# Kernel tuning notes

Hardware: AMD Instinct MI355X
Metric: run time of the kernel (lower is better)

Reference implementation:

```python
import jax, jax.numpy as jnp
import numpy as np

D = 2048          # latent_dim
H = 4096          # hrm_hidden_dim
K = 4             # hrm_update_interval
MAX_STEPS = 64    # hrm_max_steps
MOM = 0.9         # hrm_momentum
THR = 0.01        # hrm_convergence_threshold


def _gru(x, h, Wih, Whh, bih, bhh):
    # PyTorch GRUCell, gate order r, z, n
    gi = Wih @ x + bih
    gh = Whh @ h + bhh
    ir, iz, inn = jnp.split(gi, 3)
    hr, hz, hn = jnp.split(gh, 3)
    r = jax.nn.sigmoid(ir + hr)
    z = jax.nn.sigmoid(iz + hz)
    n = jnp.tanh(inn + r * hn)
    return (1.0 - z) * n + z * h


def setup_inputs() -> dict:
    key = jax.random.key(0)
    ks = jax.random.split(key, 11)
    f32 = jnp.float32
    def w(k, shape, fan):
        # scaled init (~= torch default 1/sqrt(fan)) so sigmoids/tanh stay in range
        return jax.random.normal(k, shape, f32) / np.float32(np.sqrt(fan))
    return {
        "query":   jax.random.normal(ks[0], (D,), f32),
        "hg_Wih":  w(ks[1], (3 * H, 2 * D), 2 * D),
        "hg_Whh":  w(ks[2], (3 * H, H), H),
        "hg_bih":  jnp.zeros((3 * H,), f32),
        "hg_bhh":  jnp.zeros((3 * H,), f32),
        "hd_W":    w(ks[3], (D, H), H),
        "hd_b":    jnp.zeros((D,), f32),
        "hc_W":    w(ks[4], (1, H), H),
        "hc_b":    jnp.zeros((1,), f32),
        "lg_Wih":  w(ks[5], (3 * D, D), D),
        "lg_Whh":  w(ks[6], (3 * D, D), D),
        "lg_bih":  jnp.zeros((3 * D,), f32),
        "lg_bhh":  jnp.zeros((3 * D,), f32),
        "lo_W":    w(ks[7], (D, D), D),
        "lo_b":    jnp.zeros((D,), f32),
        "halt_W":  w(ks[8], (1, H + D), H + D),
        "halt_b":  jnp.zeros((1,), f32),
        "reset_W": w(ks[9], (1, H + D + 1), H + D + 1),
        "reset_b": jnp.zeros((1,), f32),
        "li_W":    w(ks[10], (D, H), H),
        "li_b":    jnp.zeros((D,), f32),
    }


def reference(query, hg_Wih, hg_Whh, hg_bih, hg_bhh, hd_W, hd_b, hc_W, hc_b,
              lg_Wih, lg_Whh, lg_bih, lg_bhh, lo_W, lo_b,
              halt_W, halt_b, reset_W, reset_b, li_W, li_b):
    q = query[:D]  # reason() truncates/pads flattened query to D

    def step_fn(carry, step):
        h, l, cum, result, rw, mom, best, active, last_res = carry
        # H-module update every K steps (gated by 'active' = not yet halted)
        upd = active & (step % K == 0)
        h_new = _gru(jnp.concatenate([q, l]), h, hg_Wih, hg_Whh, hg_bih, hg_bhh)
        h = jnp.where(upd, h_new, h)
        directive = jnp.tanh(hd_W @ h + hd_b)
        raw_conv = jax.nn.sigmoid(hc_W @ h + hc_b)[0]
        mom = jnp.where(active, MOM * mom + (1.0 - MOM) * raw_conv, mom)
        conv = mom
        # L-module update every step
        l_new = _gru(directive, l, lg_Wih, lg_Whh, lg_bih, lg_bhh)
        l = jnp.where(active, l_new, l)
        res = jnp.tanh(lo_W @ l + lo_b)
        # ACT halting
        halt = jax.nn.sigmoid(halt_W @ jnp.concatenate([h, l]) + halt_b)[0]
        p = jnp.where(active, jnp.minimum(halt, 1.0 - cum), 0.0)
        result = result + p * res
        rw = rw + p
        cum = cum + p
        best = jnp.where(active & (conv > best + THR), conv, best)
        converged = cum > 0.95
        # learned reset (only if not converged this step, and step > K)
        reset_in = jnp.concatenate([h, l, conv[None]])
        reset_p = jax.nn.sigmoid(reset_W @ reset_in + reset_b)[0]
        do_reset = active & (~converged) & (reset_p > 0.7) & (step > K)
        l = jnp.where(do_reset, jnp.tanh(li_W @ h + li_b), l)
        last_res = jnp.where(active, res, last_res)
        active = active & (~converged)
        return (h, l, cum, result, rw, mom, best, active, last_res), None

    f32 = jnp.float32
    init = (jnp.zeros((H,), f32), jnp.zeros((D,), f32), jnp.float32(0.0),
            jnp.zeros((D,), f32), jnp.float32(0.0), jnp.float32(0.0),
            jnp.float32(0.0), jnp.array(True), jnp.zeros((D,), f32))
    (h, l, cum, result, rw, mom, best, active, last_res), _ = jax.lax.scan(
        step_fn, init, jnp.arange(MAX_STEPS))
    # final normalization: result / clamp(result_weight, 1e-8), fallback to last res
    out = jnp.where(rw > 0.0, result / jnp.maximum(rw, 1e-8), last_res)
    return out
```

## Files before the change

### kernel.cpp

```cpp
#include <hip/hip_runtime.h>

static constexpr int D = 2048;
static constexpr int H = 4096;
static constexpr int KSTEP = 4;
static constexpr int MAX_STEPS = 64;
static constexpr float MOMC = 0.9f;

static constexpr int GRID = 256;
static constexpr int BLOCK = 512;

static constexpr int BAR_OFF_FLOATS = 57344;

struct Params {
  const float* query;
  const float* hg_Wih; const float* hg_Whh; const float* hg_bih; const float* hg_bhh;
  const float* hd_W; const float* hd_b;
  const float* hc_W; const float* hc_b;
  const float* lg_Wih; const float* lg_Whh; const float* lg_bih; const float* lg_bhh;
  const float* lo_W; const float* lo_b;
  const float* halt_W; const float* halt_b;
  const float* reset_W; const float* reset_b;
  const float* li_W; const float* li_b;
  float* ws; float* out;
};

__device__ __forceinline__ float sigmoidf_(float x) { return 1.f / (1.f + expf(-x)); }

__device__ __forceinline__ void cstore(float* p, float v) {
  __hip_atomic_store(p, v, __ATOMIC_RELAXED, __HIP_MEMORY_SCOPE_AGENT);
}
__device__ __forceinline__ float cload(const float* p) {
  return __hip_atomic_load(p, __ATOMIC_RELAXED, __HIP_MEMORY_SCOPE_AGENT);
}

__device__ __forceinline__ void gridbar(unsigned* bar, unsigned& mygen) {
  __syncthreads();
  if (threadIdx.x == 0) {
    unsigned* leaf = bar + (blockIdx.x & 15) * 32;
    unsigned* root = bar + 16 * 32;
    unsigned* gen  = bar + 17 * 32;
    const unsigned leafcnt = gridDim.x >> 4;
    const unsigned want = mygen + 1;
    unsigned old = __hip_atomic_fetch_add(leaf, 1u, __ATOMIC_RELEASE, __HIP_MEMORY_SCOPE_AGENT);
    if (old == leafcnt - 1u) {
      __hip_atomic_store(leaf, 0u, __ATOMIC_RELAXED, __HIP_MEMORY_SCOPE_AGENT);
      unsigned ro = __hip_atomic_fetch_add(root, 1u, __ATOMIC_ACQ_REL, __HIP_MEMORY_SCOPE_AGENT);
      if (ro == 15u) {
        __hip_atomic_store(root, 0u, __ATOMIC_RELAXED, __HIP_MEMORY_SCOPE_AGENT);
        __hip_atomic_store(gen, want, __ATOMIC_RELEASE, __HIP_MEMORY_SCOPE_AGENT);
      } else {
        while (__hip_atomic_load(gen, __ATOMIC_RELAXED, __HIP_MEMORY_SCOPE_AGENT) != want)
          __builtin_amdgcn_s_sleep(2);
      }
    } else {
      while (__hip_atomic_load(gen, __ATOMIC_RELAXED, __HIP_MEMORY_SCOPE_AGENT) != want)
        __builtin_amdgcn_s_sleep(2);
    }
  }
  mygen += 1;
  __syncthreads();
}

__device__ __forceinline__ float wred(float v) {
  #pragma unroll
  for (int off = 1; off < 64; off <<= 1) v += __shfl_xor(v, off, 64);
  return v;
}

__device__ __forceinline__ float dot8(const float* __restrict__ row,
                                      const float* __restrict__ vec, int lane) {
  float4 a[8];
  #pragma unroll
  for (int g = 0; g < 8; ++g)
    a[g] = *reinterpret_cast<const float4*>(row + g * 256 + lane * 4);
  float s0 = 0.f, s1 = 0.f, s2 = 0.f, s3 = 0.f;
  #pragma unroll
  for (int g = 0; g < 8; g += 4) {
    float4 b0 = *reinterpret_cast<const float4*>(vec + (g + 0) * 256 + lane * 4);
    float4 b1 = *reinterpret_cast<const float4*>(vec + (g + 1) * 256 + lane * 4);
    float4 b2 = *reinterpret_cast<const float4*>(vec + (g + 2) * 256 + lane * 4);
    float4 b3 = *reinterpret_cast<const float4*>(vec + (g + 3) * 256 + lane * 4);
    s0 = fmaf(a[g+0].x, b0.x, s0); s0 = fmaf(a[g+0].y, b0.y, s0);
    s0 = fmaf(a[g+0].z, b0.z, s0); s0 = fmaf(a[g+0].w, b0.w, s0);
    s1 = fmaf(a[g+1].x, b1.x, s1); s1 = fmaf(a[g+1].y, b1.y, s1);
    s1 = fmaf(a[g+1].z, b1.z, s1); s1 = fmaf(a[g+1].w, b1.w, s1);
    s2 = fmaf(a[g+2].x, b2.x, s2); s2 = fmaf(a[g+2].y, b2.y, s2);
    s2 = fmaf(a[g+2].z, b2.z, s2); s2 = fmaf(a[g+2].w, b2.w, s2);
    s3 = fmaf(a[g+3].x, b3.x, s3); s3 = fmaf(a[g+3].y, b3.y, s3);
    s3 = fmaf(a[g+3].w, b3.w, s3); s3 = fmaf(a[g+3].z, b3.z, s3);
  }
  return (s0 + s1) + (s2 + s3);
}

__device__ __forceinline__ void dot8x2(const float* __restrict__ r0,
                                       const float* __restrict__ r1,
                                       const float* __restrict__ vec,
                                       int lane, float& o0, float& o1) {
  float4 a[8], c[8];
  #pragma unroll
  for (int g = 0; g < 8; ++g)
    a[g] = *reinterpret_cast<const float4*>(r0 + g * 256 + lane * 4);
  #pragma unroll
  for (int g = 0; g < 8; ++g)
    c[g] = *reinterpret_cast<const float4*>(r1 + g * 256 + lane * 4);
  float s0 = 0.f, s1 = 0.f, s2 = 0.f, s3 = 0.f;
  float t0 = 0.f, t1 = 0.f, t2 = 0.f, t3 = 0.f;
  #pragma unroll
  for (int g = 0; g < 8; g += 4) {
    float4 b0 = *reinterpret_cast<const float4*>(vec + (g + 0) * 256 + lane * 4);
    float4 b1 = *reinterpret_cast<const float4*>(vec + (g + 1) * 256 + lane * 4);
    float4 b2 = *reinterpret_cast<const float4*>(vec + (g + 2) * 256 + lane * 4);
    float4 b3 = *reinterpret_cast<const float4*>(vec + (g + 3) * 256 + lane * 4);
    s0 = fmaf(a[g+0].x, b0.x, s0); s0 = fmaf(a[g+0].y, b0.y, s0);
    s0 = fmaf(a[g+0].z, b0.z, s0); s0 = fmaf(a[g+0].w, b0.w, s0);
    s1 = fmaf(a[g+1].x, b1.x, s1); s1 = fmaf(a[g+1].y, b1.y, s1);
    s1 = fmaf(a[g+1].z, b1.z, s1); s1 = fmaf(a[g+1].w, b1.w, s1);
    s2 = fmaf(a[g+2].x, b2.x, s2); s2 = fmaf(a[g+2].y, b2.y, s2);
    s2 = fmaf(a[g+2].z, b2.z, s2); s2 = fmaf(a[g+2].w, b2.w, s2);
    s3 = fmaf(a[g+3].x, b3.x, s3); s3 = fmaf(a[g+3].y, b3.y, s3);
    s3 = fmaf(a[g+3].z, b3.z, s3); s3 = fmaf(a[g+3].w, b3.w, s3);
    t0 = fmaf(c[g+0].x, b0.x, t0); t0 = fmaf(c[g+0].y, b0.y, t0);
    t0 = fmaf(c[g+0].z, b0.z, t0); t0 = fmaf(c[g+0].w, b0.w, t0);
    t1 = fmaf(c[g+1].x, b1.x, t1); t1 = fmaf(c[g+1].y, b1.y, t1);
    t1 = fmaf(c[g+1].z, b1.z, t1); t1 = fmaf(c[g+1].w, b1.w, t1);
    t2 = fmaf(c[g+2].x, b2.x, t2); t2 = fmaf(c[g+2].y, b2.y, t2);
    t2 = fmaf(c[g+2].z, b2.z, t2); t2 = fmaf(c[g+2].w, b2.w, t2);
    t3 = fmaf(c[g+3].x, b3.x, t3); t3 = fmaf(c[g+3].y, b3.y, t3);
    t3 = fmaf(c[g+3].z, b3.z, t3); t3 = fmaf(c[g+3].w, b3.w, t3);
  }
  o0 = (s0 + s1) + (s2 + s3);
  o1 = (t0 + t1) + (t2 + t3);
}

__device__ __forceinline__ float dot16(const float* __restrict__ row,
                                       const float* __restrict__ vec, int lane) {
  float4 a[16];
  #pragma unroll
  for (int g = 0; g < 16; ++g)
    a[g] = *reinterpret_cast<const float4*>(row + g * 256 + lane * 4);
  float s0 = 0.f, s1 = 0.f, s2 = 0.f, s3 = 0.f;
  #pragma unroll
  for (int g = 0; g < 16; g += 4) {
    float4 b0 = *reinterpret_cast<const float4*>(vec + (g + 0) * 256 + lane * 4);
    float4 b1 = *reinterpret_cast<const float4*>(vec + (g + 1) * 256 + lane * 4);
    float4 b2 = *reinterpret_cast<const float4*>(vec + (g + 2) * 256 + lane * 4);
    float4 b3 = *reinterpret_cast<const float4*>(vec + (g + 3) * 256 + lane * 4);
    s0 = fmaf(a[g+0].x, b0.x, s0); s0 = fmaf(a[g+0].y, b0.y, s0);
    s0 = fmaf(a[g+0].z, b0.z, s0); s0 = fmaf(a[g+0].w, b0.w, s0);
    s1 = fmaf(a[g+1].x, b1.x, s1); s1 = fmaf(a[g+1].y, b1.y, s1);
    s1 = fmaf(a[g+1].z, b1.z, s1); s1 = fmaf(a[g+1].w, b1.w, s1);
    s2 = fmaf(a[g+2].x, b2.x, s2); s2 = fmaf(a[g+2].y, b2.y, s2);
    s2 = fmaf(a[g+2].z, b2.z, s2); s2 = fmaf(a[g+2].w, b2.w, s2);
    s3 = fmaf(a[g+3].x, b3.x, s3); s3 = fmaf(a[g+3].y, b3.y, s3);
    s3 = fmaf(a[g+3].z, b3.z, s3); s3 = fmaf(a[g+3].w, b3.w, s3);
  }
  return (s0 + s1) + (s2 + s3);
}

__global__ void __launch_bounds__(BLOCK, 2) reasoning_kernel(Params p) {
  const int tid = blockIdx.x * blockDim.x + threadIdx.x;
  const int nth = gridDim.x * blockDim.x;
  const int lane = threadIdx.x & 63;
  const int wid = threadIdx.x >> 6;
  const int gw = tid >> 6;
  const int nw = nth >> 6;

  __shared__ __align__(16) float sh_h[H];
  __shared__ __align__(16) float sh_l[D];
  __shared__ __align__(16) float sh_dir[D];
  __shared__ float sh_red[32];

  float* qc   = p.ws;
  float* gi_l = qc + 3 * H;
  float* ghh  = gi_l + 3 * H;
  float* ghl2 = ghh + 3 * H;
  float* gil  = ghl2 + 6 * D;
  float* dirv = gil + 3 * D;
  unsigned* bar = (unsigned*)(p.ws + BAR_OFF_FLOATS);

  for (int j = threadIdx.x; j < H; j += blockDim.x) sh_h[j] = 0.f;
  for (int j = threadIdx.x; j < D; j += blockDim.x) sh_l[j] = 0.f;
  __syncthreads();

  float cum = 0.f, rw = 0.f, mom = 0.f;
  float rawconv = 0.f, halt_h = 0.f, reset_h = 0.f;
  float sum0 = 0.f, sum1 = 0.f;
  const bool owner = (gw < D / 2);
  unsigned mygen = 0;

  for (int step = 0; step < MAX_STEPS; ++step) {
    const int par = step & 1;
    const bool upd = (step & 3) == 0;
    float* ghl = ghl2 + par * 3 * D;

    if (upd) {
      if (step == 0) {
        for (int t = gw * 2; t < 3 * H; t += nw * 2) {
          float o0, o1;
          dot8x2(p.hg_Wih + (size_t)t * (2 * D),
                 p.hg_Wih + (size_t)(t + 1) * (2 * D), p.query, lane, o0, o1);
          o0 = wred(o0); o1 = wred(o1);
          if (lane == 0) { cstore(qc + t, o0); cstore(qc + t + 1, o1); }
        }
      } else {
        for (int t = gw * 2; t < 3 * H; t += nw * 2) {
          float o0, o1;
          dot8x2(p.hg_Wih + (size_t)t * (2 * D) + D,
                 p.hg_Wih + (size_t)(t + 1) * (2 * D) + D, sh_l, lane, o0, o1);
          o0 = wred(o0); o1 = wred(o1);
          if (lane == 0) { cstore(gi_l + t, o0); cstore(gi_l + t + 1, o1); }
        }
        for (int t = gw; t < 3 * H; t += nw) {
          float s = wred(dot16(p.hg_Whh + (size_t)t * H, sh_h, lane));
          if (lane == 0) cstore(ghh + t, s + p.hg_bhh[t]);
        }
        for (int t = gw * 2; t < 2 * D; t += nw * 2) {
          float o0, o1;
          dot8x2(p.lg_Whh + (size_t)t * D,
                 p.lg_Whh + (size_t)(t + 1) * D, sh_l, lane, o0, o1);
          o0 = wred(o0); o1 = wred(o1);
          if (lane == 0) { cstore(ghl + t, o0 + p.lg_bhh[t]); cstore(ghl + t + 1, o1 + p.lg_bhh[t + 1]); }
        }
        for (int t = 2 * D + gw; t < 3 * D; t += nw) {
          float s = wred(dot8(p.lg_Whh + (size_t)t * D, sh_l, lane));
          if (lane == 0) cstore(ghl + t, s + p.lg_bhh[t]);
        }
      }
    } else {
      for (int t = gw * 2; t < 2 * D; t += nw * 2) {
        float o0, o1;
        dot8x2(p.lg_Whh + (size_t)t * D,
               p.lg_Whh + (size_t)(t + 1) * D, sh_l, lane, o0, o1);
        o0 = wred(o0); o1 = wred(o1);
        if (lane == 0) { cstore(ghl + t, o0 + p.lg_bhh[t]); cstore(ghl + t + 1, o1 + p.lg_bhh[t + 1]); }
      }
      for (int t = 2 * D + gw; t < 3 * D; t += nw) {
        float s = wred(dot8(p.lg_Whh + (size_t)t * D, sh_l, lane));
        if (lane == 0) cstore(ghl + t, s + p.lg_bhh[t]);
      }
    }
    gridbar(bar, mygen);

    if (upd) {
      if (step == 0) {
        for (int i = threadIdx.x; i < H; i += blockDim.x) {
          float r = sigmoidf_(cload(qc + i) + p.hg_bih[i] + p.hg_bhh[i]);
          float z = sigmoidf_(cload(qc + H + i) + p.hg_bih[H + i] + p.hg_bhh[H + i]);
          float n = tanhf(cload(qc + 2 * H + i) + p.hg_bih[2 * H + i] + r * p.hg_bhh[2 * H + i]);
          sh_h[i] = (1.f - z) * n;
        }
      } else {
        for (int i = threadIdx.x; i < H; i += blockDim.x) {
          float r = sigmoidf_(cload(qc + i) + cload(gi_l + i) + p.hg_bih[i] + cload(ghh + i));
          float z = sigmoidf_(cload(qc + H + i) + cload(gi_l + H + i) + p.hg_bih[H + i] + cload(ghh + H + i));
          float n = tanhf(cload(qc + 2 * H + i) + cload(gi_l + 2 * H + i) + p.hg_bih[2 * H + i]
                          + r * cload(ghh + 2 * H + i));
          sh_h[i] = (1.f - z) * n + z * sh_h[i];
        }
      }
      __syncthreads();

      {
        float a0 = 0.f, a1 = 0.f, a2 = 0.f;
        for (int k = threadIdx.x; k < H; k += BLOCK) {
          float hv = sh_h[k];
          a0 = fmaf(p.hc_W[k], hv, a0);
          a1 = fmaf(p.halt_W[k], hv, a1);
          a2 = fmaf(p.reset_W[k], hv, a2);
        }
        a0 = wred(a0); a1 = wred(a1); a2 = wred(a2);
        if (lane == 0) { sh_red[wid] = a0; sh_red[8 + wid] = a1; sh_red[16 + wid] = a2; }
        __syncthreads();
        float t0 = 0.f, t1 = 0.f, t2 = 0.f;
        #pragma unroll
        for (int w = 0; w < 8; ++w) { t0 += sh_red[w]; t1 += sh_red[8 + w]; t2 += sh_red[16 + w]; }
        rawconv = sigmoidf_(t0 + p.hc_b[0]);
        halt_h = t1; reset_h = t2;
        __syncthreads();
      }

      for (int t = gw; t < D; t += nw) {
        float s = wred(dot16(p.hd_W + (size_t)t * H, sh_h, lane));
        if (lane == 0) cstore(dirv + t, tanhf(s + p.hd_b[t]));
      }
      gridbar(bar, mygen);

      for (int j = threadIdx.x; j < D; j += blockDim.x) sh_dir[j] = cload(dirv + j);
      __syncthreads();

      for (int t = gw * 2; t < 2 * D; t += nw * 2) {
        float o0, o1;
        dot8x2(p.lg_Wih + (size_t)t * D,
               p.lg_Wih + (size_t)(t + 1) * D, sh_dir, lane, o0, o1);
        o0 = wred(o0); o1 = wred(o1);
        if (lane == 0) { cstore(gil + t, o0 + p.lg_bih[t]); cstore(gil + t + 1, o1 + p.lg_bih[t + 1]); }
      }
      for (int t = 2 * D + gw; t < 3 * D; t += nw) {
        float s = wred(dot8(p.lg_Wih + (size_t)t * D, sh_dir, lane));
        if (lane == 0) cstore(gil + t, s + p.lg_bih[t]);
      }
      gridbar(bar, mygen);
    }

    if (step == 0) {
      for (int j = threadIdx.x; j < D; j += blockDim.x) {
        float r = sigmoidf_(cload(gil + j) + p.lg_bhh[j]);
        float z = sigmoidf_(cload(gil + D + j) + p.lg_bhh[D + j]);
        float n = tanhf(cload(gil + 2 * D + j) + r * p.lg_bhh[2 * D + j]);
        sh_l[j] = (1.f - z) * n;
      }
    } else {
      for (int j = threadIdx.x; j < D; j += blockDim.x) {
        float r = sigmoidf_(cload(gil + j) + cload(ghl + j));
        float z = sigmoidf_(cload(gil + D + j) + cload(ghl + D + j));
        float n = tanhf(cload(gil + 2 * D + j) + r * cload(ghl + 2 * D + j));
        sh_l[j] = (1.f - z) * n + z * sh_l[j];
      }
    }
    __syncthreads();

    float halt_l, reset_l;
    {
      float a0 = 0.f, a1 = 0.f;
      for (int k = threadIdx.x; k < D; k += BLOCK) {
        float lv = sh_l[k];
        a0 = fmaf(p.halt_W[H + k], lv, a0);
        a1 = fmaf(p.reset_W[H + k], lv, a1);
      }
      a0 = wred(a0); a1 = wred(a1);
      if (lane == 0) { sh_red[wid] = a0; sh_red[8 + wid] = a1; }
      __syncthreads();
      float t0 = 0.f, t1 = 0.f;
      #pragma unroll
      for (int w = 0; w < 8; ++w) { t0 += sh_red[w]; t1 += sh_red[8 + w]; }
      halt_l = t0; reset_l = t1;
      __syncthreads();
    }

    mom = MOMC * mom + (1.f - MOMC) * rawconv;
    float halt = sigmoidf_(halt_h + halt_l + p.halt_b[0]);
    float pp = fminf(halt, 1.f - cum);
    cum += pp; rw += pp;
    bool converged = cum > 0.95f;

    if (owner) {
      int t = gw * 2;
      float o0, o1;
      dot8x2(p.lo_W + (size_t)t * D, p.lo_W + (size_t)(t + 1) * D, sh_l, lane, o0, o1);
      o0 = wred(o0); o1 = wred(o1);
      sum0 += pp * tanhf(o0 + p.lo_b[t]);
      sum1 += pp * tanhf(o1 + p.lo_b[t + 1]);
    }
    if (converged) break;

    float reset_p = sigmoidf_(reset_h + reset_l + p.reset_W[H + D] * mom + p.reset_b[0]);
    if ((reset_p > 0.7f) && (step > KSTEP)) {
      for (int t = gw; t < D; t += nw) {
        float s = wred(dot16(p.li_W + (size_t)t * H, sh_h, lane));
        if (lane == 0) cstore(dirv + t, tanhf(s + p.li_b[t]));
      }
      gridbar(bar, mygen);
      for (int j = threadIdx.x; j < D; j += blockDim.x) sh_l[j] = cload(dirv + j);
      __syncthreads();
    }
  }

  if (owner && lane == 0) {
    float inv = 1.f / fmaxf(rw, 1e-8f);
    p.out[2 * gw]     = sum0 * inv;
    p.out[2 * gw + 1] = sum1 * inv;
  }
}

extern "C" void kernel_launch(void* const* d_in, const int* in_sizes, int n_in,
                              void* d_out, int out_size, void* d_ws, size_t ws_size,
                              hipStream_t stream) {
  Params prm;
  prm.query   = (const float*)d_in[0];
  prm.hg_Wih  = (const float*)d_in[1];
  prm.hg_Whh  = (const float*)d_in[2];
  prm.hg_bih  = (const float*)d_in[3];
  prm.hg_bhh  = (const float*)d_in[4];
  prm.hd_W    = (const float*)d_in[5];
  prm.hd_b    = (const float*)d_in[6];
  prm.hc_W    = (const float*)d_in[7];
  prm.hc_b    = (const float*)d_in[8];
  prm.lg_Wih  = (const float*)d_in[9];
  prm.lg_Whh  = (const float*)d_in[10];
  prm.lg_bih  = (const float*)d_in[11];
  prm.lg_bhh  = (const float*)d_in[12];
  prm.lo_W    = (const float*)d_in[13];
  prm.lo_b    = (const float*)d_in[14];
  prm.halt_W  = (const float*)d_in[15];
  prm.halt_b  = (const float*)d_in[16];
  prm.reset_W = (const float*)d_in[17];
  prm.reset_b = (const float*)d_in[18];
  prm.li_W    = (const float*)d_in[19];
  prm.li_b    = (const float*)d_in[20];
  prm.ws  = (float*)d_ws;
  prm.out = (float*)d_out;

  hipMemsetAsync((char*)d_ws + (size_t)BAR_OFF_FLOATS * sizeof(float), 0, 4096, stream);

  void* args[] = { &prm };
  const int grids[3] = { GRID, GRID / 2, GRID / 4 };
  for (int g = 0; g < 3; ++g) {
    hipError_t e = hipLaunchCooperativeKernel((const void*)reasoning_kernel,
                                              dim3(grids[g]), dim3(BLOCK),
                                              args, 0, stream);
    if (e == hipSuccess) break;
  }
}
```

Measured before the change: 117.7 us.

## Raise block size to 768 and reassign lo_W rows per block

Raises the block to 768 threads with a minimum of 3 blocks in the launch bounds, which gives more waves per block on the persistent grid. The separate tail loops for the third GRU gate are folded into the paired dot8x2 loops, which now run over all 3*D rows. The lo_W output projection moves from a per-global-warp ownership scheme to a per-block row split, so the first 8 waves of each block handle D/grid rows each. The tighter register budget per thread can cause spills, and the per-block output mapping assumes the grid divides D evenly.

```diff
diff --git a/kernel.cpp b/kernel.cpp
--- a/kernel.cpp
+++ b/kernel.cpp
@@ -7,7 +7,7 @@
 static constexpr float MOMC = 0.9f;
 
 static constexpr int GRID = 256;
-static constexpr int BLOCK = 512;
+static constexpr int BLOCK = 768;
 
 static constexpr int BAR_OFF_FLOATS = 57344;
 
@@ -87,7 +87,7 @@
     s2 = fmaf(a[g+2].x, b2.x, s2); s2 = fmaf(a[g+2].y, b2.y, s2);
     s2 = fmaf(a[g+2].z, b2.z, s2); s2 = fmaf(a[g+2].w, b2.w, s2);
     s3 = fmaf(a[g+3].x, b3.x, s3); s3 = fmaf(a[g+3].y, b3.y, s3);
-    s3 = fmaf(a[g+3].w, b3.w, s3); s3 = fmaf(a[g+3].z, b3.z, s3);
+    s3 = fmaf(a[g+3].z, b3.z, s3); s3 = fmaf(a[g+3].w, b3.w, s3);
   }
   return (s0 + s1) + (s2 + s3);
 }
@@ -157,7 +157,7 @@
   return (s0 + s1) + (s2 + s3);
 }
 
-__global__ void __launch_bounds__(BLOCK, 2) reasoning_kernel(Params p) {
+__global__ void __launch_bounds__(BLOCK, 3) reasoning_kernel(Params p) {
   const int tid = blockIdx.x * blockDim.x + threadIdx.x;
   const int nth = gridDim.x * blockDim.x;
   const int lane = threadIdx.x & 63;
@@ -168,7 +168,7 @@
   __shared__ __align__(16) float sh_h[H];
   __shared__ __align__(16) float sh_l[D];
   __shared__ __align__(16) float sh_dir[D];
-  __shared__ float sh_red[32];
+  __shared__ float sh_red[48];
 
   float* qc   = p.ws;
   float* gi_l = qc + 3 * H;
@@ -184,8 +184,9 @@
 
   float cum = 0.f, rw = 0.f, mom = 0.f;
   float rawconv = 0.f, halt_h = 0.f, reset_h = 0.f;
-  float sum0 = 0.f, sum1 = 0.f;
-  const bool owner = (gw < D / 2);
+  const int rpb = D / gridDim.x;
+  const int rpb8 = rpb >> 3;
+  float sums[4] = {0.f, 0.f, 0.f, 0.f};
   unsigned mygen = 0;
 
   for (int step = 0; step < MAX_STEPS; ++step) {
@@ -214,29 +215,21 @@
           float s = wred(dot16(p.hg_Whh + (size_t)t * H, sh_h, lane));
           if (lane == 0) cstore(ghh + t, s + p.hg_bhh[t]);
         }
-        for (int t = gw * 2; t < 2 * D; t += nw * 2) {
+        for (int t = gw * 2; t < 3 * D; t += nw * 2) {
           float o0, o1;
           dot8x2(p.lg_Whh + (size_t)t * D,
                  p.lg_Whh + (size_t)(t + 1) * D, sh_l, lane, o0, o1);
           o0 = wred(o0); o1 = wred(o1);
           if (lane == 0) { cstore(ghl + t, o0 + p.lg_bhh[t]); cstore(ghl + t + 1, o1 + p.lg_bhh[t + 1]); }
         }
-        for (int t = 2 * D + gw; t < 3 * D; t += nw) {
-          float s = wred(dot8(p.lg_Whh + (size_t)t * D, sh_l, lane));
-          if (lane == 0) cstore(ghl + t, s + p.lg_bhh[t]);
-        }
       }
     } else {
-      for (int t = gw * 2; t < 2 * D; t += nw * 2) {
+      for (int t = gw * 2; t < 3 * D; t += nw * 2) {
         float o0, o1;
         dot8x2(p.lg_Whh + (size_t)t * D,
                p.lg_Whh + (size_t)(t + 1) * D, sh_l, lane, o0, o1);
         o0 = wred(o0); o1 = wred(o1);
         if (lane == 0) { cstore(ghl + t, o0 + p.lg_bhh[t]); cstore(ghl + t + 1, o1 + p.lg_bhh[t + 1]); }
-      }
-      for (int t = 2 * D + gw; t < 3 * D; t += nw) {
-        float s = wred(dot8(p.lg_Whh + (size_t)t * D, sh_l, lane));
-        if (lane == 0) cstore(ghl + t, s + p.lg_bhh[t]);
       }
     }
     gridbar(bar, mygen);
@@ -269,11 +262,11 @@
           a2 = fmaf(p.reset_W[k], hv, a2);
         }
         a0 = wred(a0); a1 = wred(a1); a2 = wred(a2);
-        if (lane == 0) { sh_red[wid] = a0; sh_red[8 + wid] = a1; sh_red[16 + wid] = a2; }
+        if (lane == 0) { sh_red[wid] = a0; sh_red[12 + wid] = a1; sh_red[24 + wid] = a2; }
         __syncthreads();
         float t0 = 0.f, t1 = 0.f, t2 = 0.f;
         #pragma unroll
-        for (int w = 0; w < 8; ++w) { t0 += sh_red[w]; t1 += sh_red[8 + w]; t2 += sh_red[16 + w]; }
+        for (int w = 0; w < 12; ++w) { t0 += sh_red[w]; t1 += sh_red[12 + w]; t2 += sh_red[24 + w]; }
         rawconv = sigmoidf_(t0 + p.hc_b[0]);
         halt_h = t1; reset_h = t2;
         __syncthreads();
@@ -288,16 +281,12 @@
       for (int j = threadIdx.x; j < D; j += blockDim.x) sh_dir[j] = cload(dirv + j);
       __syncthreads();
 
-      for (int t = gw * 2; t < 2 * D; t += nw * 2) {
+      for (int t = gw * 2; t < 3 * D; t += nw * 2) {
         float o0, o1;
         dot8x2(p.lg_Wih + (size_t)t * D,
                p.lg_Wih + (size_t)(t + 1) * D, sh_dir, lane, o0, o1);
         o0 = wred(o0); o1 = wred(o1);
         if (lane == 0) { cstore(gil + t, o0 + p.lg_bih[t]); cstore(gil + t + 1, o1 + p.lg_bih[t + 1]); }
-      }
-      for (int t = 2 * D + gw; t < 3 * D; t += nw) {
-        float s = wred(dot8(p.lg_Wih + (size_t)t * D, sh_dir, lane));
-        if (lane == 0) cstore(gil + t, s + p.lg_bih[t]);
       }
       gridbar(bar, mygen);
     }
@@ -328,11 +317,11 @@
         a1 = fmaf(p.reset_W[H + k], lv, a1);
       }
       a0 = wred(a0); a1 = wred(a1);
-      if (lane == 0) { sh_red[wid] = a0; sh_red[8 + wid] = a1; }
+      if (lane == 0) { sh_red[wid] = a0; sh_red[12 + wid] = a1; }
       __syncthreads();
       float t0 = 0.f, t1 = 0.f;
       #pragma unroll
-      for (int w = 0; w < 8; ++w) { t0 += sh_red[w]; t1 += sh_red[8 + w]; }
+      for (int w = 0; w < 12; ++w) { t0 += sh_red[w]; t1 += sh_red[12 + w]; }
       halt_l = t0; reset_l = t1;
       __syncthreads();
     }
@@ -343,13 +332,15 @@
     cum += pp; rw += pp;
     bool converged = cum > 0.95f;
 
-    if (owner) {
-      int t = gw * 2;
-      float o0, o1;
-      dot8x2(p.lo_W + (size_t)t * D, p.lo_W + (size_t)(t + 1) * D, sh_l, lane, o0, o1);
-      o0 = wred(o0); o1 = wred(o1);
-      sum0 += pp * tanhf(o0 + p.lo_b[t]);
-      sum1 += pp * tanhf(o1 + p.lo_b[t + 1]);
+    if (wid < 8) {
+      #pragma unroll
+      for (int k = 0; k < 4; ++k) {
+        if (k < rpb8) {
+          int row = blockIdx.x * rpb + wid + 8 * k;
+          float s = wred(dot8(p.lo_W + (size_t)row * D, sh_l, lane));
+          sums[k] += pp * tanhf(s + p.lo_b[row]);
+        }
+      }
     }
     if (converged) break;
 
@@ -365,10 +356,15 @@
     }
   }
 
-  if (owner && lane == 0) {
+  if (wid < 8 && lane == 0) {
     float inv = 1.f / fmaxf(rw, 1e-8f);
-    p.out[2 * gw]     = sum0 * inv;
-    p.out[2 * gw + 1] = sum1 * inv;
+    #pragma unroll
+    for (int k = 0; k < 4; ++k) {
+      if (k < rpb8) {
+        int row = blockIdx.x * rpb + wid + 8 * k;
+        p.out[row] = sums[k] * inv;
+      }
+    }
   }
 }
 
```

Measured after the change: 142.4 us. +21.0%, slower.
